# Performance work log

Hardware: AMD Instinct MI355X
Metric: run time of the kernel (lower is better)

Reference implementation:

```python
import jax, jax.numpy as jnp
import numpy as np

HEADS = 8
DIM_HEAD = 64
SCALE = DIM_HEAD ** -0.5


def setup_inputs() -> dict:
    key = jax.random.key(0)
    ks = jax.random.split(key, 6)
    B, N, M = 4, 4096, 1024
    QD, CD, ID = 320, 768, 512
    s = lambda d: (1.0 / np.sqrt(d)).astype(np.float32)
    return {
        "x": jax.random.normal(ks[0], (B, N, QD), dtype=jnp.float32),
        "context": jax.random.normal(ks[1], (B, M, CD), dtype=jnp.float32),
        "Wq": jax.random.normal(ks[2], (QD, ID), dtype=jnp.float32) * s(QD),
        "Wk": jax.random.normal(ks[3], (CD, ID), dtype=jnp.float32) * s(CD),
        "Wv": jax.random.normal(ks[4], (CD, ID), dtype=jnp.float32) * s(CD),
        "Wo": jax.random.normal(ks[5], (ID, QD), dtype=jnp.float32) * s(ID),
        "bo": jnp.zeros((QD,), dtype=jnp.float32),
    }


def reference(x, context, Wq, Wk, Wv, Wo, bo):
    B, N, _ = x.shape
    M = context.shape[1]
    # projections
    q = (x @ Wq).reshape(B, N, HEADS, DIM_HEAD)        # b n h d
    k = (context @ Wk).reshape(B, M, HEADS, DIM_HEAD)  # b m h d
    v = (context @ Wv).reshape(B, M, HEADS, DIM_HEAD)
    # scaled dot-product attention per head
    scores = jnp.einsum("bnhd,bmhd->bhnm", q, k) * SCALE
    attn = jax.nn.softmax(scores, axis=-1)
    out = jnp.einsum("bhnm,bmhd->bnhd", attn, v).reshape(B, N, HEADS * DIM_HEAD)
    # output projection (dropout p=0.0 is identity)
    return out @ Wo + bo
```

## Files before the change

kernel.cpp:

```cpp
#include <hip/hip_runtime.h>
#include <cmath>

constexpr int BATCH  = 4;
constexpr int SEQ_N  = 4096;
constexpr int SEQ_M  = 1024;
constexpr int QD     = 320;
constexpr int CD     = 768;
constexpr int ID     = 512;
constexpr float QFOLD = 0.125f * 1.44269504f;
constexpr float EK2F  = -8.0f * 1.44269504f;

typedef __bf16 bf16x8 __attribute__((ext_vector_type(8)));
typedef __bf16 bf16x4 __attribute__((ext_vector_type(4)));
typedef __bf16 bf16x2 __attribute__((ext_vector_type(2)));
typedef float  f32x4  __attribute__((ext_vector_type(4)));

__device__ __forceinline__ void gload_lds16(const __bf16* g, __bf16* l) {
    __builtin_amdgcn_global_load_lds(
        (const __attribute__((address_space(1))) void*)g,
        (__attribute__((address_space(3))) void*)l, 16, 0, 0);
}

__global__ __launch_bounds__(256)
void cvt_all(const float* __restrict__ x, const float* __restrict__ ctx,
             const float* __restrict__ Wq, const float* __restrict__ Wk,
             const float* __restrict__ Wv, const float* __restrict__ Wo,
             __bf16* __restrict__ xb, __bf16* __restrict__ ctxb,
             __bf16* __restrict__ WqT, __bf16* __restrict__ WkT,
             __bf16* __restrict__ WvT, __bf16* __restrict__ WoT) {
    __shared__ float tile[32][33];
    int bid = blockIdx.x;
    if (bid < 4096) {
        constexpr int NX8 = SEQ_N * BATCH * QD / 8;
        int i = bid * 256 + threadIdx.x;
        const float* s; __bf16* d; int j;
        if (i < NX8) { s = x; d = xb; j = i; }
        else         { s = ctx; d = ctxb; j = i - NX8; }
        const float4* sp = reinterpret_cast<const float4*>(s) + (size_t)j * 2;
        float4 a = sp[0], b = sp[1];
        bf16x8 o = { (__bf16)a.x, (__bf16)a.y, (__bf16)a.z, (__bf16)a.w,
                     (__bf16)b.x, (__bf16)b.y, (__bf16)b.z, (__bf16)b.w };
        reinterpret_cast<bf16x8*>(d)[j] = o;
        return;
    }
    int wb = bid - 4096;
    const float* W; __bf16* WT; int K, N, tid; float scl = 1.0f;
    if (wb < 160)      { W = Wq; WT = WqT; K = 320; N = 512; tid = wb; scl = QFOLD; }
    else if (wb < 544) { W = Wk; WT = WkT; K = 768; N = 512; tid = wb - 160; }
    else if (wb < 928) { W = Wv; WT = WvT; K = 768; N = 512; tid = wb - 544; }
    else               { W = Wo; WT = WoT; K = 512; N = 320; tid = wb - 928; }
    int kt = K / 32;
    int k0 = (tid % kt) * 32, n0 = (tid / kt) * 32;
    int tc = threadIdx.x & 31, tr = threadIdx.x >> 5;
#pragma unroll
    for (int p = 0; p < 4; ++p)
        tile[p * 8 + tr][tc] = W[(size_t)(k0 + p * 8 + tr) * N + n0 + tc];
    __syncthreads();
#pragma unroll
    for (int p = 0; p < 4; ++p)
        WT[(size_t)(n0 + p * 8 + tr) * K + k0 + tc] = (__bf16)(tile[tc][p * 8 + tr] * scl);
}

__global__ __launch_bounds__(256)
void gemm_kv(const __bf16* __restrict__ A, const __bf16* __restrict__ BT,
             __bf16* __restrict__ Kb, __bf16* __restrict__ Vt, int M, int K) {
    __shared__ __attribute__((aligned(16))) __bf16 sA[2][64][64];
    __shared__ __attribute__((aligned(16))) __bf16 sB[2][64][64];

    const int t = threadIdx.x;
    const int wave = t >> 6, lane = t & 63;
    const int q = lane >> 4, c = lane & 15;
    const int wm = wave >> 1, wn = wave & 1;
    const int row0 = blockIdx.x * 64, col0 = blockIdx.y * 64;
    const int srow = lane >> 3, sch = lane & 7;
    const int fch = sch ^ srow;

    auto stage = [&](int buf, int k0) {
#pragma unroll
        for (int i = 0; i < 2; ++i) {
            int r = wave * 16 + i * 8;
            gload_lds16(A + (size_t)(row0 + r + srow) * K + k0 + fch * 8,
                        &sA[buf][r][0] + lane * 8);
            gload_lds16(BT + (size_t)(col0 + r + srow) * K + k0 + fch * 8,
                        &sB[buf][r][0] + lane * 8);
        }
    };

    f32x4 acc[2][2] = {};
    stage(0, 0);
    const int iters = K >> 6;
    for (int it = 0; it < iters; ++it) {
        const int p = it & 1;
        __syncthreads();
        if (it + 1 < iters) stage(p ^ 1, (it + 1) * 64);
#pragma unroll
        for (int ks = 0; ks < 2; ++ks) {
            const int so = ((ks * 4 + q) ^ (c & 7)) * 8;
            bf16x8 am[2], bn[2];
#pragma unroll
            for (int i = 0; i < 2; ++i)
                am[i] = *reinterpret_cast<const bf16x8*>(&sA[p][wm * 32 + i * 16 + c][0] + so);
#pragma unroll
            for (int j = 0; j < 2; ++j)
                bn[j] = *reinterpret_cast<const bf16x8*>(&sB[p][wn * 32 + j * 16 + c][0] + so);
#pragma unroll
            for (int i = 0; i < 2; ++i)
#pragma unroll
                for (int j = 0; j < 2; ++j)
                    acc[i][j] = __builtin_amdgcn_mfma_f32_16x16x32_bf16(bn[j], am[i], acc[i][j], 0, 0, 0);
        }
    }

    if (blockIdx.y < 8) {
#pragma unroll
        for (int i = 0; i < 2; ++i)
#pragma unroll
            for (int j = 0; j < 2; ++j) {
                int mrow = row0 + wm * 32 + i * 16 + c;
                int ncol = col0 + wn * 32 + j * 16 + q * 4;
                bf16x4 v = { (__bf16)acc[i][j][0], (__bf16)acc[i][j][1],
                             (__bf16)acc[i][j][2], (__bf16)acc[i][j][3] };
                *reinterpret_cast<bf16x4*>(&Kb[(size_t)mrow * 512 + ncol]) = v;
            }
    } else {
        __bf16* ldsT = (__bf16*)sA;
        __syncthreads();
#pragma unroll
        for (int i = 0; i < 2; ++i)
#pragma unroll
            for (int j = 0; j < 2; ++j) {
                int ml = wm * 32 + i * 16 + c;
                int dl = wn * 32 + j * 16 + q * 4;
#pragma unroll
                for (int r = 0; r < 4; ++r)
                    ldsT[(dl + r) * 72 + ml] = (__bf16)acc[i][j][r];
            }
        __syncthreads();
        int b = row0 >> 10, m0 = row0 & 1023;
        int h = (col0 - 512) >> 6;
        int d = t >> 2, ch = t & 3;
        __bf16* dst = Vt + (((size_t)((b * 8 + h) * 64 + d)) << 10) + m0 + ch * 16;
        const __bf16* src = &ldsT[d * 72 + ch * 16];
        *reinterpret_cast<bf16x8*>(dst)     = *reinterpret_cast<const bf16x8*>(src);
        *reinterpret_cast<bf16x8*>(dst + 8) = *reinterpret_cast<const bf16x8*>(src + 8);
    }
}

__global__ __launch_bounds__(256, 2)
void flash_attn(const __bf16* __restrict__ xb, const __bf16* __restrict__ WqT,
                const __bf16* __restrict__ Kb, const __bf16* __restrict__ Vt,
                __bf16* __restrict__ AO) {
    __shared__ __attribute__((aligned(16))) __bf16 smem[34816];
    __bf16* sPT = smem + 16384;

    const int t = threadIdx.x;
    const int wave = t >> 6, lane = t & 63;
    const int q = lane >> 4, c = lane & 15;
    const int bh = blockIdx.y;
    const int b = bh >> 3, h = bh & 7;
    const int n0 = blockIdx.x * 256;
    const int srow = lane >> 3, sch = lane & 7;
    const int fch = sch ^ srow;

    f32x4 accQ[4][4] = {};
    {
        __bf16* sX = smem;
        __bf16* sW = smem + 16384;
        for (int k0 = 0; k0 < QD; k0 += 64) {
            __syncthreads();
#pragma unroll
            for (int i = 0; i < 8; ++i) {
                int r = wave * 64 + i * 8;
                gload_lds16(xb + (size_t)(b * SEQ_N + n0 + r + srow) * QD + k0 + fch * 8,
                            sX + r * 64 + lane * 8);
            }
#pragma unroll
            for (int i = 0; i < 2; ++i) {
                int r = wave * 16 + i * 8;
                gload_lds16(WqT + (size_t)(h * 64 + r + srow) * QD + k0 + fch * 8,
                            sW + r * 64 + lane * 8);
            }
            __syncthreads();
#pragma unroll
            for (int ks = 0; ks < 2; ++ks) {
                const int so = ((ks * 4 + q) ^ (c & 7)) * 8;
                bf16x8 aw[4], bx[4];
#pragma unroll
                for (int dt = 0; dt < 4; ++dt)
                    aw[dt] = *reinterpret_cast<const bf16x8*>(sW + (dt * 16 + c) * 64 + so);
#pragma unroll
                for (int qt = 0; qt < 4; ++qt)
                    bx[qt] = *reinterpret_cast<const bf16x8*>(sX + (wave * 64 + qt * 16 + c) * 64 + so);
#pragma unroll
                for (int dt = 0; dt < 4; ++dt)
#pragma unroll
                    for (int qt = 0; qt < 4; ++qt)
                        accQ[dt][qt] = __builtin_amdgcn_mfma_f32_16x16x32_bf16(aw[dt], bx[qt], accQ[dt][qt], 0, 0, 0);
            }
        }
    }
    __syncthreads();

    __bf16* sQw = sPT + wave * 4608;
#pragma unroll
    for (int dt = 0; dt < 4; ++dt)
#pragma unroll
        for (int qt = 0; qt < 4; ++qt) {
            bf16x2 w0 = { (__bf16)accQ[dt][qt][0], (__bf16)accQ[dt][qt][1] };
            bf16x2 w1 = { (__bf16)accQ[dt][qt][2], (__bf16)accQ[dt][qt][3] };
            __bf16* pr = sQw + (qt * 16 + c) * 72 + dt * 16 + q * 4;
            *reinterpret_cast<bf16x2*>(pr)     = w0;
            *reinterpret_cast<bf16x2*>(pr + 2) = w1;
        }
    bf16x8 aq[4][2];
#pragma unroll
    for (int qt = 0; qt < 4; ++qt)
#pragma unroll
        for (int ks = 0; ks < 2; ++ks)
            aq[qt][ks] = *reinterpret_cast<const bf16x8*>(sQw + (qt * 16 + c) * 72 + ks * 32 + q * 8);

    auto stageKV = [&](int buf, int m0) {
        __bf16* sK = smem + buf * 8192;
        __bf16* sV = smem + buf * 8192 + 4096;
#pragma unroll
        for (int i = 0; i < 2; ++i) {
            int r = wave * 16 + i * 8;
            gload_lds16(Kb + (size_t)(b * SEQ_M + m0 + r + srow) * ID + h * 64 + fch * 8,
                        sK + r * 64 + lane * 8);
            gload_lds16(Vt + (((size_t)((b * 8 + h) * 64 + r + srow)) << 10) + m0 + fch * 8,
                        sV + r * 64 + lane * 8);
        }
    };

    const bf16x8 ONES = { (__bf16)1.0f, (__bf16)1.0f, (__bf16)1.0f, (__bf16)1.0f,
                          (__bf16)1.0f, (__bf16)1.0f, (__bf16)1.0f, (__bf16)1.0f };
    f32x4 accO[4][4] = {};
    f32x4 accL[4] = {};

    stageKV(0, 0);
    constexpr int TILES = SEQ_M / 64;
    for (int mt = 0; mt < TILES; ++mt) {
        const int p = mt & 1;
        __syncthreads();
        if (mt + 1 < TILES) stageKV(p ^ 1, (mt + 1) * 64);
        const __bf16* sK = smem + p * 8192;
        const __bf16* sV = smem + p * 8192 + 4096;

        f32x4 s[4][4];
#pragma unroll
        for (int qt = 0; qt < 4; ++qt)
#pragma unroll
            for (int ct = 0; ct < 4; ++ct)
                s[qt][ct] = f32x4{ EK2F, EK2F, EK2F, EK2F };
#pragma unroll
        for (int ks = 0; ks < 2; ++ks) {
            const int so = ((ks * 4 + q) ^ (c & 7)) * 8;
#pragma unroll
            for (int ct = 0; ct < 4; ++ct) {
                bf16x8 ak = *reinterpret_cast<const bf16x8*>(sK + (ct * 16 + c) * 64 + so);
#pragma unroll
                for (int qt = 0; qt < 4; ++qt)
                    s[qt][ct] = __builtin_amdgcn_mfma_f32_16x16x32_bf16(ak, aq[qt][ks], s[qt][ct], 0, 0, 0);
            }
        }

#pragma unroll
        for (int qt = 0; qt < 4; ++qt)
#pragma unroll
            for (int ct = 0; ct < 4; ++ct) {
                float p0 = exp2f(s[qt][ct][0]);
                float p1 = exp2f(s[qt][ct][1]);
                float p2 = exp2f(s[qt][ct][2]);
                float p3 = exp2f(s[qt][ct][3]);
                bf16x2 w0 = { (__bf16)p0, (__bf16)p1 };
                bf16x2 w1 = { (__bf16)p2, (__bf16)p3 };
                __bf16* pr = sQw + (qt * 16 + c) * 72 + ct * 16 + q * 4;
                *reinterpret_cast<bf16x2*>(pr)     = w0;
                *reinterpret_cast<bf16x2*>(pr + 2) = w1;
            }

#pragma unroll
        for (int ks = 0; ks < 2; ++ks) {
            const int so = ((ks * 4 + q) ^ (c & 7)) * 8;
            bf16x8 bp[4];
#pragma unroll
            for (int qt = 0; qt < 4; ++qt)
                bp[qt] = *reinterpret_cast<const bf16x8*>(sQw + (qt * 16 + c) * 72 + ks * 32 + q * 8);
#pragma unroll
            for (int qt = 0; qt < 4; ++qt)
                accL[qt] = __builtin_amdgcn_mfma_f32_16x16x32_bf16(ONES, bp[qt], accL[qt], 0, 0, 0);
#pragma unroll
            for (int nt = 0; nt < 4; ++nt) {
                bf16x8 av = *reinterpret_cast<const bf16x8*>(sV + (nt * 16 + c) * 64 + so);
#pragma unroll
                for (int qt = 0; qt < 4; ++qt)
                    accO[qt][nt] = __builtin_amdgcn_mfma_f32_16x16x32_bf16(av, bp[qt], accO[qt][nt], 0, 0, 0);
            }
        }
    }

#pragma unroll
    for (int qt = 0; qt < 4; ++qt) {
        float inv = 1.0f / accL[qt][0];
        size_t rowb = (size_t)(b * SEQ_N + n0 + wave * 64 + qt * 16 + c) * ID + h * 64;
#pragma unroll
        for (int nt = 0; nt < 4; ++nt) {
            bf16x4 v = { (__bf16)(accO[qt][nt][0] * inv), (__bf16)(accO[qt][nt][1] * inv),
                         (__bf16)(accO[qt][nt][2] * inv), (__bf16)(accO[qt][nt][3] * inv) };
            *reinterpret_cast<bf16x4*>(&AO[rowb + nt * 16 + q * 4]) = v;
        }
    }
}

__global__ __launch_bounds__(256)
void gemm_out(const __bf16* __restrict__ A, const __bf16* __restrict__ BT,
              const float* __restrict__ bias, float* __restrict__ C,
              int M, int N, int K) {
    __shared__ __attribute__((aligned(16))) __bf16 sA[2][128][64];
    __shared__ __attribute__((aligned(16))) __bf16 sB[2][64][64];

    const int t = threadIdx.x;
    const int wave = t >> 6, lane = t & 63;
    const int q = lane >> 4, c = lane & 15;
    const int wm = wave >> 1, wn = wave & 1;
    const int row0 = blockIdx.x * 128, col0 = blockIdx.y * 64;
    const int srow = lane >> 3, sch = lane & 7;
    const int fch = sch ^ srow;

    auto stage = [&](int buf, int k0) {
#pragma unroll
        for (int i = 0; i < 4; ++i) {
            int r = wave * 32 + i * 8;
            gload_lds16(A + (size_t)(row0 + r + srow) * K + k0 + fch * 8,
                        &sA[buf][r][0] + lane * 8);
        }
#pragma unroll
        for (int i = 0; i < 2; ++i) {
            int r = wave * 16 + i * 8;
            gload_lds16(BT + (size_t)(col0 + r + srow) * K + k0 + fch * 8,
                        &sB[buf][r][0] + lane * 8);
        }
    };

    f32x4 acc[4][2] = {};
    stage(0, 0);
    const int iters = K >> 6;
    for (int it = 0; it < iters; ++it) {
        const int p = it & 1;
        __syncthreads();
        if (it + 1 < iters) stage(p ^ 1, (it + 1) * 64);
#pragma unroll
        for (int ks = 0; ks < 2; ++ks) {
            const int so = ((ks * 4 + q) ^ (c & 7)) * 8;
            bf16x8 am[4], bn[2];
#pragma unroll
            for (int i = 0; i < 4; ++i)
                am[i] = *reinterpret_cast<const bf16x8*>(&sA[p][wm * 64 + i * 16 + c][0] + so);
#pragma unroll
            for (int j = 0; j < 2; ++j)
                bn[j] = *reinterpret_cast<const bf16x8*>(&sB[p][wn * 32 + j * 16 + c][0] + so);
#pragma unroll
            for (int i = 0; i < 4; ++i)
#pragma unroll
                for (int j = 0; j < 2; ++j)
                    acc[i][j] = __builtin_amdgcn_mfma_f32_16x16x32_bf16(bn[j], am[i], acc[i][j], 0, 0, 0);
        }
    }

#pragma unroll
    for (int i = 0; i < 4; ++i)
#pragma unroll
        for (int j = 0; j < 2; ++j) {
            int mrow = row0 + wm * 64 + i * 16 + c;
            int ncol = col0 + wn * 32 + j * 16 + q * 4;
            float4 v = { acc[i][j][0] + bias[ncol + 0],
                         acc[i][j][1] + bias[ncol + 1],
                         acc[i][j][2] + bias[ncol + 2],
                         acc[i][j][3] + bias[ncol + 3] };
            *reinterpret_cast<float4*>(&C[(size_t)mrow * N + ncol]) = v;
        }
}

extern "C" void kernel_launch(void* const* d_in, const int* in_sizes, int n_in,
                              void* d_out, int out_size, void* d_ws, size_t ws_size,
                              hipStream_t stream) {
    const float* x   = (const float*)d_in[0];
    const float* ctx = (const float*)d_in[1];
    const float* Wq  = (const float*)d_in[2];
    const float* Wk  = (const float*)d_in[3];
    const float* Wv  = (const float*)d_in[4];
    const float* Wo  = (const float*)d_in[5];
    const float* bo  = (const float*)d_in[6];
    float* out = (float*)d_out;

    char* ws = (char*)d_ws;
    __bf16* xb   = (__bf16*)(ws + 0);
    __bf16* ctxb = (__bf16*)(ws + 10485760);
    __bf16* AO   = (__bf16*)(ws + 16777216);
    __bf16* Kb   = (__bf16*)(ws + 33554432);
    __bf16* Vt   = (__bf16*)(ws + 37748736);
    __bf16* WqT  = (__bf16*)(ws + 41943040);
    __bf16* WkT  = (__bf16*)(ws + 42270720);
    __bf16* WvT  = (__bf16*)(ws + 43057152);
    __bf16* WoT  = (__bf16*)(ws + 43843584);

    const int MX = BATCH * SEQ_N;
    const int MC = BATCH * SEQ_M;
    dim3 blk(256);

    cvt_all<<<dim3(5184), blk, 0, stream>>>(x, ctx, Wq, Wk, Wv, Wo,
                                            xb, ctxb, WqT, WkT, WvT, WoT);

    gemm_kv<<<dim3(MC / 64, 16), blk, 0, stream>>>(ctxb, WkT, Kb, Vt, MC, CD);

    flash_attn<<<dim3(SEQ_N / 256, 32), blk, 0, stream>>>(xb, WqT, Kb, Vt, AO);

    gemm_out<<<dim3(MX / 128, QD / 64), blk, 0, stream>>>(AO, WoT, bo, out, MX, QD, ID);
}
```

Before: 173.9 us.

## Keep softmax probabilities in registers via permuted K rows, drop LDS round-trip

After: 154.7 us. 11.0% less time.

```diff
diff --git a/kernel.cpp b/kernel.cpp
--- a/kernel.cpp
+++ b/kernel.cpp
@@ -19,6 +19,14 @@
     __builtin_amdgcn_global_load_lds(
         (const __attribute__((address_space(1))) void*)g,
         (__attribute__((address_space(3))) void*)l, 16, 0, 0);
+}
+
+__device__ __forceinline__ float fast_exp2(float x) {
+#if __has_builtin(__builtin_amdgcn_exp2f)
+    return __builtin_amdgcn_exp2f(x);
+#else
+    return exp2f(x);
+#endif
 }
 
 __global__ __launch_bounds__(256)
@@ -150,8 +158,7 @@
 void flash_attn(const __bf16* __restrict__ xb, const __bf16* __restrict__ WqT,
                 const __bf16* __restrict__ Kb, const __bf16* __restrict__ Vt,
                 __bf16* __restrict__ AO) {
-    __shared__ __attribute__((aligned(16))) __bf16 smem[34816];
-    __bf16* sPT = smem + 16384;
+    __shared__ __attribute__((aligned(16))) __bf16 smem[20480];
 
     const int t = threadIdx.x;
     const int wave = t >> 6, lane = t & 63;
@@ -201,7 +208,7 @@
     }
     __syncthreads();
 
-    __bf16* sQw = sPT + wave * 4608;
+    __bf16* sQw = smem + wave * 4608;
 #pragma unroll
     for (int dt = 0; dt < 4; ++dt)
 #pragma unroll
@@ -218,6 +225,7 @@
 #pragma unroll
         for (int ks = 0; ks < 2; ++ks)
             aq[qt][ks] = *reinterpret_cast<const bf16x8*>(sQw + (qt * 16 + c) * 72 + ks * 32 + q * 8);
+    __syncthreads();
 
     auto stageKV = [&](int buf, int m0) {
         __bf16* sK = smem + buf * 8192;
@@ -225,17 +233,19 @@
 #pragma unroll
         for (int i = 0; i < 2; ++i) {
             int r = wave * 16 + i * 8;
-            gload_lds16(Kb + (size_t)(b * SEQ_M + m0 + r + srow) * ID + h * 64 + fch * 8,
+            int rho = r + srow;
+            int kl = (rho & 32) | (((rho & 15) >> 2) << 3)
+                   | (rho & 3) | (((rho >> 4) & 1) << 2);
+            gload_lds16(Kb + (size_t)(b * SEQ_M + m0 + kl) * ID + h * 64 + fch * 8,
                         sK + r * 64 + lane * 8);
-            gload_lds16(Vt + (((size_t)((b * 8 + h) * 64 + r + srow)) << 10) + m0 + fch * 8,
+            gload_lds16(Vt + (((size_t)((b * 8 + h) * 64 + rho)) << 10) + m0 + fch * 8,
                         sV + r * 64 + lane * 8);
         }
     };
 
-    const bf16x8 ONES = { (__bf16)1.0f, (__bf16)1.0f, (__bf16)1.0f, (__bf16)1.0f,
-                          (__bf16)1.0f, (__bf16)1.0f, (__bf16)1.0f, (__bf16)1.0f };
+    const f32x4 ekc = { EK2F, EK2F, EK2F, EK2F };
     f32x4 accO[4][4] = {};
-    f32x4 accL[4] = {};
+    float psum[4] = {};
 
     stageKV(0, 0);
     constexpr int TILES = SEQ_M / 64;
@@ -248,11 +258,6 @@
 
         f32x4 s[4][4];
 #pragma unroll
-        for (int qt = 0; qt < 4; ++qt)
-#pragma unroll
-            for (int ct = 0; ct < 4; ++ct)
-                s[qt][ct] = f32x4{ EK2F, EK2F, EK2F, EK2F };
-#pragma unroll
         for (int ks = 0; ks < 2; ++ks) {
             const int so = ((ks * 4 + q) ^ (c & 7)) * 8;
 #pragma unroll
@@ -260,48 +265,52 @@
                 bf16x8 ak = *reinterpret_cast<const bf16x8*>(sK + (ct * 16 + c) * 64 + so);
 #pragma unroll
                 for (int qt = 0; qt < 4; ++qt)
-                    s[qt][ct] = __builtin_amdgcn_mfma_f32_16x16x32_bf16(ak, aq[qt][ks], s[qt][ct], 0, 0, 0);
-            }
-        }
-
-#pragma unroll
-        for (int qt = 0; qt < 4; ++qt)
-#pragma unroll
-            for (int ct = 0; ct < 4; ++ct) {
-                float p0 = exp2f(s[qt][ct][0]);
-                float p1 = exp2f(s[qt][ct][1]);
-                float p2 = exp2f(s[qt][ct][2]);
-                float p3 = exp2f(s[qt][ct][3]);
-                bf16x2 w0 = { (__bf16)p0, (__bf16)p1 };
-                bf16x2 w1 = { (__bf16)p2, (__bf16)p3 };
-                __bf16* pr = sQw + (qt * 16 + c) * 72 + ct * 16 + q * 4;
-                *reinterpret_cast<bf16x2*>(pr)     = w0;
-                *reinterpret_cast<bf16x2*>(pr + 2) = w1;
-            }
+                    s[qt][ct] = (ks == 0)
+                        ? __builtin_amdgcn_mfma_f32_16x16x32_bf16(ak, aq[qt][0], ekc, 0, 0, 0)
+                        : __builtin_amdgcn_mfma_f32_16x16x32_bf16(ak, aq[qt][1], s[qt][ct], 0, 0, 0);
+            }
+        }
+
+        bf16x8 bp[4][2];
+#pragma unroll
+        for (int qt = 0; qt < 4; ++qt) {
+            float pp[16];
+#pragma unroll
+            for (int ct = 0; ct < 4; ++ct)
+#pragma unroll
+                for (int r = 0; r < 4; ++r)
+                    pp[ct * 4 + r] = fast_exp2(s[qt][ct][r]);
+#pragma unroll
+            for (int g = 0; g < 2; ++g)
+                bp[qt][g] = bf16x8{ (__bf16)pp[g * 8 + 0], (__bf16)pp[g * 8 + 1],
+                                    (__bf16)pp[g * 8 + 2], (__bf16)pp[g * 8 + 3],
+                                    (__bf16)pp[g * 8 + 4], (__bf16)pp[g * 8 + 5],
+                                    (__bf16)pp[g * 8 + 6], (__bf16)pp[g * 8 + 7] };
+            psum[qt] += (((pp[0] + pp[1]) + (pp[2] + pp[3])) +
+                         ((pp[4] + pp[5]) + (pp[6] + pp[7]))) +
+                        (((pp[8] + pp[9]) + (pp[10] + pp[11])) +
+                         ((pp[12] + pp[13]) + (pp[14] + pp[15])));
+        }
 
 #pragma unroll
         for (int ks = 0; ks < 2; ++ks) {
             const int so = ((ks * 4 + q) ^ (c & 7)) * 8;
-            bf16x8 bp[4];
-#pragma unroll
-            for (int qt = 0; qt < 4; ++qt)
-                bp[qt] = *reinterpret_cast<const bf16x8*>(sQw + (qt * 16 + c) * 72 + ks * 32 + q * 8);
-#pragma unroll
-            for (int qt = 0; qt < 4; ++qt)
-                accL[qt] = __builtin_amdgcn_mfma_f32_16x16x32_bf16(ONES, bp[qt], accL[qt], 0, 0, 0);
 #pragma unroll
             for (int nt = 0; nt < 4; ++nt) {
                 bf16x8 av = *reinterpret_cast<const bf16x8*>(sV + (nt * 16 + c) * 64 + so);
 #pragma unroll
                 for (int qt = 0; qt < 4; ++qt)
-                    accO[qt][nt] = __builtin_amdgcn_mfma_f32_16x16x32_bf16(av, bp[qt], accO[qt][nt], 0, 0, 0);
+                    accO[qt][nt] = __builtin_amdgcn_mfma_f32_16x16x32_bf16(av, bp[qt][ks], accO[qt][nt], 0, 0, 0);
             }
         }
     }
 
 #pragma unroll
     for (int qt = 0; qt < 4; ++qt) {
-        float inv = 1.0f / accL[qt][0];
+        float l = psum[qt];
+        l += __shfl_xor(l, 16);
+        l += __shfl_xor(l, 32);
+        float inv = 1.0f / l;
         size_t rowb = (size_t)(b * SEQ_N + n0 + wave * 64 + qt * 16 + c) * ID + h * 64;
 #pragma unroll
         for (int nt = 0; nt < 4; ++nt) {
```
